# Kernel optimization log

Measured on AMD Instinct MI355X. Metric: run time of the kernel, lower is better.

Reference implementation:

```python
import jax, jax.numpy as jnp
import numpy as np

CAPACITY_FACTOR = 1.25


def setup_inputs() -> dict:
    key = jax.random.key(0)
    ks = jax.random.split(key, 5)
    B, N, D, E, H = 4, 2048, 1024, 8, 4096
    x = jax.random.normal(ks[0], (B, N, D), dtype=jnp.float32)
    w_router = jax.random.normal(ks[1], (D, E), dtype=jnp.float32) * 0.02
    w1 = jax.random.normal(ks[2], (E, D, H), dtype=jnp.float32) * 0.02
    b1 = jnp.zeros((E, H), dtype=jnp.float32)
    w2 = jax.random.normal(ks[3], (E, H, D), dtype=jnp.float32) * 0.02
    b2 = jnp.zeros((E, D), dtype=jnp.float32)
    return {"x": x, "w_router": w_router, "w1": w1, "b1": b1, "w2": w2, "b2": b2}


def reference(x, w_router, w1, b1, w2, b2):
    B, N, D = x.shape
    E = w_router.shape[1]
    C = int(N * CAPACITY_FACTOR // E)  # expert capacity

    # ---- top-1 switch router ----
    logits = jnp.einsum('bnd,de->bne', x, w_router)                 # [B,N,E]
    z = jax.nn.logsumexp(logits, axis=-1)                           # [B,N]
    router_z_loss = jnp.mean(z * z)
    probs = jax.nn.softmax(logits, axis=-1)                         # [B,N,E]
    gate = jnp.max(probs, axis=-1)                                  # [B,N]
    idx = jnp.argmax(probs, axis=-1)                                # [B,N]
    mask = jax.nn.one_hot(idx, E, dtype=x.dtype)                    # [B,N,E]

    # load-balancing aux loss (Switch-Transformer style)
    density = jnp.mean(mask, axis=1)                                # [B,E] fraction routed
    density_proxy = jnp.mean(probs, axis=1)                         # [B,E] mean router prob
    aux_loss = jnp.mean(jnp.sum(density * density_proxy, axis=-1)) * (E * E)

    # position within each expert; drop tokens beyond capacity
    pos = jnp.cumsum(mask, axis=1) - 1.0                            # [B,N,E]
    pos = pos.astype(jnp.int32)
    # one_hot zeros out indices outside [0,C); mask zeros unrouted slots
    dispatch = mask[..., None] * jax.nn.one_hot(pos, C, dtype=x.dtype)  # [B,N,E,C]
    combine = dispatch * gate[:, :, None, None]                     # [B,N,E,C]

    # ---- dense dispatch -> grouped expert FFN -> dense combine ----
    expert_inputs = jnp.einsum('bnd,bnec->becd', x, dispatch)       # [B,E,C,D]
    h = jax.nn.gelu(jnp.einsum('becd,edh->bech', expert_inputs, w1)
                    + b1[None, :, None, :])                          # [B,E,C,H]
    expert_outputs = jnp.einsum('bech,ehd->becd', h, w2) + b2[None, :, None, :]
    output = jnp.einsum('becd,bnec->bnd', expert_outputs, combine)  # [B,N,D]
    return output, aux_loss, router_z_loss
```

## Files before the change

### kernel.cpp

```cpp
#include <hip/hip_runtime.h>
#include <hip/hip_bf16.h>
#include <math.h>

#define B_ 4
#define N_ 2048
#define D_ 1024
#define E_ 8
#define H_ 4096
#define C_ 320
#define M_ (B_*C_)

typedef __attribute__((ext_vector_type(8))) short short8;
typedef __attribute__((ext_vector_type(4))) float floatx4;

__device__ __forceinline__ unsigned short f2bf(float f) {
  unsigned u = __builtin_bit_cast(unsigned, f);
  u += 0x7fffu + ((u >> 16) & 1u);
  return (unsigned short)(u >> 16);
}

__device__ __forceinline__ float gelu_fast(float x) {
  float u = 0.7978845608028654f * (x + 0.044715f * x * x * x);
  float t = 1.f - 2.f / (__expf(2.f * u) + 1.f);
  return 0.5f * x * (1.f + t);
}

__device__ __forceinline__ void gload_lds16(const unsigned short* g, unsigned short* l) {
  __builtin_amdgcn_global_load_lds(
      (const __attribute__((address_space(1))) unsigned int*)g,
      (__attribute__((address_space(3))) unsigned int*)l, 16, 0, 0);
}

__global__ __launch_bounds__(256) void router_kernel(
    const float* __restrict__ x, const float* __restrict__ wr,
    int* __restrict__ idx_buf, float* __restrict__ gate_buf,
    float* __restrict__ stats)
{
  int lane  = threadIdx.x & 63;
  int wave  = threadIdx.x >> 6;
  int token = blockIdx.x * 4 + wave;
  int b     = token >> 11;

  const float* xp = x + (size_t)token * D_ + lane * 16;
  float xv[16];
#pragma unroll
  for (int i = 0; i < 4; i++) {
    float4 v = ((const float4*)xp)[i];
    xv[i*4+0]=v.x; xv[i*4+1]=v.y; xv[i*4+2]=v.z; xv[i*4+3]=v.w;
  }
  double acc[8];
#pragma unroll
  for (int e = 0; e < 8; e++) acc[e] = 0.0;
  const float* wp = wr + (size_t)(lane * 16) * E_;
#pragma unroll
  for (int i = 0; i < 16; i++) {
    float xs = xv[i];
#pragma unroll
    for (int e = 0; e < 8; e++) acc[e] += (double)xs * (double)wp[i*8 + e];
  }
  for (int off = 32; off > 0; off >>= 1) {
#pragma unroll
    for (int e = 0; e < 8; e++) acc[e] += __shfl_xor(acc[e], off, 64);
  }

  float l[8];
#pragma unroll
  for (int e = 0; e < 8; e++) l[e] = (float)acc[e];
  float m = l[0]; int best = 0;
#pragma unroll
  for (int e = 1; e < 8; e++) if (l[e] > m) { m = l[e]; best = e; }
  float p[8], sum = 0.f;
#pragma unroll
  for (int e = 0; e < 8; e++) { p[e] = expf(l[e] - m); sum += p[e]; }
  float inv = 1.f / sum;
#pragma unroll
  for (int e = 0; e < 8; e++) p[e] *= inv;
  float z    = m + logf(sum);
  float gate = inv;

  __shared__ float s_cnt[8], s_prox[8], s_zsq[1];
  if (threadIdx.x < 8)  { s_cnt[threadIdx.x] = 0.f; s_prox[threadIdx.x] = 0.f; }
  if (threadIdx.x == 8) s_zsq[0] = 0.f;
  __syncthreads();
  if (lane == 0) {
    idx_buf[token]  = best;
    gate_buf[token] = gate;
    atomicAdd(&s_zsq[0], z * z);
    atomicAdd(&s_cnt[best], 1.f);
#pragma unroll
    for (int e = 0; e < 8; e++) atomicAdd(&s_prox[e], p[e]);
  }
  __syncthreads();
  if (threadIdx.x < 8) {
    atomicAdd(&stats[b*8 + threadIdx.x],      s_cnt[threadIdx.x]);
    atomicAdd(&stats[32 + b*8 + threadIdx.x], s_prox[threadIdx.x]);
  }
  if (threadIdx.x == 8) atomicAdd(&stats[64], s_zsq[0]);
}

__global__ __launch_bounds__(64) void pos_kernel(
    const int* __restrict__ idx_buf, int* __restrict__ slot_token)
{
  int be = blockIdx.x;
  int b = be >> 3, e = be & 7;
  int lane = threadIdx.x;
  int base = 0;
  int* out = slot_token + (size_t)(e * B_ + b) * C_;
  for (int n0 = 0; n0 < N_; n0 += 64) {
    int n = n0 + lane;
    bool match = (idx_buf[b * N_ + n] == e);
    unsigned long long mask = __ballot(match);
    int my = base + __popcll(mask & ((1ull << lane) - 1ull));
    if (match && my < C_) out[my] = b * N_ + n;
    base += __popcll(mask);
  }
}

__global__ __launch_bounds__(256) void gather_kernel(
    const float* __restrict__ x, const int* __restrict__ slot_token,
    unsigned short* __restrict__ xe)
{
  int row = blockIdx.x;
  int t = slot_token[row];
  int col = threadIdx.x * 4;
  ushort4 o;
  if (t >= 0) {
    float4 v = *(const float4*)(x + (size_t)t * D_ + col);
    o.x = f2bf(v.x); o.y = f2bf(v.y); o.z = f2bf(v.z); o.w = f2bf(v.w);
  } else {
    o.x = 0; o.y = 0; o.z = 0; o.w = 0;
  }
  *(ushort4*)(xe + (size_t)row * D_ + col) = o;
}

__global__ __launch_bounds__(256) void transcast_kernel(
    const float* __restrict__ in, unsigned short* __restrict__ out, int R, int Cc)
{
  int e = blockIdx.z;
  const float* pin = in + (size_t)e * R * Cc;
  unsigned short* pout = out + (size_t)e * R * Cc;
  __shared__ float T[64][65];
  int r0 = blockIdx.y * 64, c0 = blockIdx.x * 64;
  {
    int row = threadIdx.x >> 2;
    int cb  = (threadIdx.x & 3) * 4;
#pragma unroll
    for (int p = 0; p < 4; p++) {
      int col = cb + p * 16;
      float4 v = *(const float4*)(pin + (size_t)(r0 + row) * Cc + c0 + col);
      T[row][col+0] = v.x; T[row][col+1] = v.y; T[row][col+2] = v.z; T[row][col+3] = v.w;
    }
  }
  __syncthreads();
  {
    int ocb = threadIdx.x >> 4;
    int or4 = (threadIdx.x & 15) * 4;
#pragma unroll
    for (int p = 0; p < 4; p++) {
      int oc = ocb + p * 16;
      ushort4 o;
      o.x = f2bf(T[or4+0][oc]); o.y = f2bf(T[or4+1][oc]);
      o.z = f2bf(T[or4+2][oc]); o.w = f2bf(T[or4+3][oc]);
      *(ushort4*)(pout + (size_t)(c0 + oc) * R + r0 + or4) = o;
    }
  }
}

template<int EPI>
__global__ __launch_bounds__(256) void gemm_kernel(
    const unsigned short* __restrict__ A,
    const unsigned short* __restrict__ BT,
    const float* __restrict__ bias,
    unsigned short* __restrict__ Hout,
    float* __restrict__ Out,
    const int* __restrict__ slot_token,
    const float* __restrict__ gate_buf,
    int M, int K, int Nn)
{
  int e  = blockIdx.z;
  int m0 = blockIdx.y * 128;
  int n0 = blockIdx.x * 128;
  const unsigned short* Ae = A  + (size_t)e * M  * K;
  const unsigned short* Be = BT + (size_t)e * Nn * K;

  __shared__ __align__(16) unsigned short As[2][128 * 32];
  __shared__ __align__(16) unsigned short Bs[2][128 * 32];
  __shared__ int   s_tok[128];
  __shared__ float s_gate[128];

  int tid  = threadIdx.x;
  int lane = tid & 63;
  int wave = tid >> 6;
  int wm   = (wave >> 1) * 64;
  int wn   = (wave & 1) * 64;
  int lr   = lane & 15;
  int quad = lane >> 4;

  if constexpr (EPI == 1) {
    if (tid < 128) {
      int t = slot_token[(size_t)e * M + m0 + tid];
      s_tok[tid]  = t;
      s_gate[tid] = (t >= 0) ? gate_buf[t] : 0.f;
    }
  }

  floatx4 acc[4][4];
#pragma unroll
  for (int i = 0; i < 4; i++)
#pragma unroll
    for (int j = 0; j < 4; j++) acc[i][j] = (floatx4){0.f, 0.f, 0.f, 0.f};

  int rA0 = wave * 32 + (lane >> 2);
  int kcc = (lane & 3) * 8;
  const unsigned short* Ag0 = Ae + (size_t)(m0 + rA0)      * K + kcc;
  const unsigned short* Ag1 = Ae + (size_t)(m0 + rA0 + 16) * K + kcc;
  const unsigned short* Bg0 = Be + (size_t)(n0 + rA0)      * K + kcc;
  const unsigned short* Bg1 = Be + (size_t)(n0 + rA0 + 16) * K + kcc;
  const unsigned offA0 = (wave * 32) * 32;
  const unsigned offA1 = (wave * 32 + 16) * 32;

  gload_lds16(Ag0, &As[0][offA0]);
  gload_lds16(Ag1, &As[0][offA1]);
  gload_lds16(Bg0, &Bs[0][offA0]);
  gload_lds16(Bg1, &Bs[0][offA1]);
  Ag0 += 32; Ag1 += 32; Bg0 += 32; Bg1 += 32;

  int nIter = K >> 5;
  int buf = 0;
  for (int it = 0; it < nIter; ++it) {
    __syncthreads();
    if (it + 1 < nIter) {
      gload_lds16(Ag0, &As[buf ^ 1][offA0]);
      gload_lds16(Ag1, &As[buf ^ 1][offA1]);
      gload_lds16(Bg0, &Bs[buf ^ 1][offA0]);
      gload_lds16(Bg1, &Bs[buf ^ 1][offA1]);
      Ag0 += 32; Ag1 += 32; Bg0 += 32; Bg1 += 32;
    }
    short8 af[4], bf[4];
#pragma unroll
    for (int i = 0; i < 4; i++) {
      af[i] = *(const short8*)(&As[buf][(wm + i * 16 + lr) * 32 + quad * 8]);
      bf[i] = *(const short8*)(&Bs[buf][(wn + i * 16 + lr) * 32 + quad * 8]);
    }
#pragma unroll
    for (int i = 0; i < 4; i++)
#pragma unroll
      for (int j = 0; j < 4; j++)
        acc[i][j] = __builtin_amdgcn_mfma_f32_16x16x32_bf16(af[i], bf[j], acc[i][j], 0, 0, 0);
    buf ^= 1;
  }

#pragma unroll
  for (int i = 0; i < 4; i++) {
    int rloc = wm + i * 16 + quad * 4;
#pragma unroll
    for (int j = 0; j < 4; j++) {
      int col = n0 + wn + j * 16 + lr;
      float bz = bias[(size_t)e * Nn + col];
      if constexpr (EPI == 0) {
        size_t base = (size_t)e * M * Nn + (size_t)(m0 + rloc) * Nn + col;
#pragma unroll
        for (int r = 0; r < 4; r++)
          Hout[base + (size_t)r * Nn] = f2bf(gelu_fast(acc[i][j][r] + bz));
      } else {
#pragma unroll
        for (int r = 0; r < 4; r++) {
          int t = s_tok[rloc + r];
          if (t >= 0)
            Out[(size_t)t * D_ + col] = s_gate[rloc + r] * (acc[i][j][r] + bz);
        }
      }
    }
  }
}

__global__ void loss_kernel(const float* __restrict__ stats, float* __restrict__ out)
{
  float aux = 0.f;
  for (int i = 0; i < 32; i++) aux += stats[i] * stats[32 + i];
  aux *= 64.f / ((float)B_ * (float)N_ * (float)N_);
  out[0] = aux;
  out[1] = stats[64] / (float)(B_ * N_);
}

extern "C" void kernel_launch(void* const* d_in, const int* in_sizes, int n_in,
                              void* d_out, int out_size, void* d_ws, size_t ws_size,
                              hipStream_t stream)
{
  (void)in_sizes; (void)n_in; (void)ws_size;
  const float* x  = (const float*)d_in[0];
  const float* wr = (const float*)d_in[1];
  const float* w1 = (const float*)d_in[2];
  const float* b1 = (const float*)d_in[3];
  const float* w2 = (const float*)d_in[4];
  const float* b2 = (const float*)d_in[5];
  float* out = (float*)d_out;

  char* ws = (char*)d_ws;
  int*   idx_buf  = (int*)(ws + 0);
  float* gate_buf = (float*)(ws + 32768);
  float* stats    = (float*)(ws + 65536);
  int*   slot_tok = (int*)(ws + 66560);
  unsigned short* xe  = (unsigned short*)(ws + 107520);
  unsigned short* wbf = (unsigned short*)(ws + 21079040);
  unsigned short* hbf = (unsigned short*)(ws + 88187904);

  hipMemsetAsync(d_out, 0, (size_t)out_size * 4, stream);
  hipMemsetAsync(stats, 0, 1024, stream);
  hipMemsetAsync(slot_tok, 0xFF, (size_t)E_ * B_ * C_ * 4, stream);

  router_kernel<<<(B_ * N_) / 4, 256, 0, stream>>>(x, wr, idx_buf, gate_buf, stats);
  pos_kernel<<<B_ * E_, 64, 0, stream>>>(idx_buf, slot_tok);
  gather_kernel<<<E_ * M_, 256, 0, stream>>>(x, slot_tok, xe);

  transcast_kernel<<<dim3(H_ / 64, D_ / 64, E_), 256, 0, stream>>>(w1, wbf, D_, H_);
  gemm_kernel<0><<<dim3(H_ / 128, M_ / 128, E_), 256, 0, stream>>>(
      xe, wbf, b1, hbf, nullptr, nullptr, nullptr, M_, D_, H_);
  transcast_kernel<<<dim3(D_ / 64, H_ / 64, E_), 256, 0, stream>>>(w2, wbf, H_, D_);
  gemm_kernel<1><<<dim3(D_ / 128, M_ / 128, E_), 256, 0, stream>>>(
      hbf, wbf, b2, nullptr, out, slot_tok, gate_buf, M_, H_, D_);

  loss_kernel<<<1, 1, 0, stream>>>(stats, out + (size_t)B_ * N_ * D_);
}
```

Baseline: 673.4 us.

## Remap GEMM grid to interleave experts and fold loss kernel into pos kernel

The GEMM launches switch from a 3D grid to a flat 1D grid. The expert index is taken from the low bits of blockIdx.x, and M tiles vary fastest within each expert. This changes block dispatch order so that all 8 experts run at once and neighbouring blocks share the same B-weight column tile, which should help L2 reuse of weights and spread work across XCDs. The separate single-thread loss kernel is merged into pos_kernel to save one launch. pos_kernel runs after router_kernel on the same stream, so the stats it reads are already complete.

```diff
diff --git a/kernel.cpp b/kernel.cpp
--- a/kernel.cpp
+++ b/kernel.cpp
@@ -99,7 +99,8 @@
 }
 
 __global__ __launch_bounds__(64) void pos_kernel(
-    const int* __restrict__ idx_buf, int* __restrict__ slot_token)
+    const int* __restrict__ idx_buf, int* __restrict__ slot_token,
+    const float* __restrict__ stats, float* __restrict__ loss_out)
 {
   int be = blockIdx.x;
   int b = be >> 3, e = be & 7;
@@ -114,6 +115,13 @@
     if (match && my < C_) out[my] = b * N_ + n;
     base += __popcll(mask);
   }
+  if (be == 0 && lane == 0) {
+    float aux = 0.f;
+    for (int i = 0; i < 32; i++) aux += stats[i] * stats[32 + i];
+    aux *= 64.f / ((float)B_ * (float)N_ * (float)N_);
+    loss_out[0] = aux;
+    loss_out[1] = stats[64] / (float)(B_ * N_);
+  }
 }
 
 __global__ __launch_bounds__(256) void gather_kernel(
@@ -175,11 +183,12 @@
     float* __restrict__ Out,
     const int* __restrict__ slot_token,
     const float* __restrict__ gate_buf,
-    int M, int K, int Nn)
-{
-  int e  = blockIdx.z;
-  int m0 = blockIdx.y * 128;
-  int n0 = blockIdx.x * 128;
+    int M, int K, int Nn, int MT)
+{
+  int e  = blockIdx.x & 7;
+  int s  = blockIdx.x >> 3;
+  int m0 = (s % MT) * 128;
+  int n0 = (s / MT) * 128;
   const unsigned short* Ae = A  + (size_t)e * M  * K;
   const unsigned short* Be = BT + (size_t)e * Nn * K;
 
@@ -274,15 +283,6 @@
   }
 }
 
-__global__ void loss_kernel(const float* __restrict__ stats, float* __restrict__ out)
-{
-  float aux = 0.f;
-  for (int i = 0; i < 32; i++) aux += stats[i] * stats[32 + i];
-  aux *= 64.f / ((float)B_ * (float)N_ * (float)N_);
-  out[0] = aux;
-  out[1] = stats[64] / (float)(B_ * N_);
-}
-
 extern "C" void kernel_launch(void* const* d_in, const int* in_sizes, int n_in,
                               void* d_out, int out_size, void* d_ws, size_t ws_size,
                               hipStream_t stream)
@@ -310,15 +310,14 @@
   hipMemsetAsync(slot_tok, 0xFF, (size_t)E_ * B_ * C_ * 4, stream);
 
   router_kernel<<<(B_ * N_) / 4, 256, 0, stream>>>(x, wr, idx_buf, gate_buf, stats);
-  pos_kernel<<<B_ * E_, 64, 0, stream>>>(idx_buf, slot_tok);
+  pos_kernel<<<B_ * E_, 64, 0, stream>>>(idx_buf, slot_tok, stats,
+                                         out + (size_t)B_ * N_ * D_);
   gather_kernel<<<E_ * M_, 256, 0, stream>>>(x, slot_tok, xe);
 
   transcast_kernel<<<dim3(H_ / 64, D_ / 64, E_), 256, 0, stream>>>(w1, wbf, D_, H_);
-  gemm_kernel<0><<<dim3(H_ / 128, M_ / 128, E_), 256, 0, stream>>>(
-      xe, wbf, b1, hbf, nullptr, nullptr, nullptr, M_, D_, H_);
+  gemm_kernel<0><<<E_ * (H_ / 128) * (M_ / 128), 256, 0, stream>>>(
+      xe, wbf, b1, hbf, nullptr, nullptr, nullptr, M_, D_, H_, M_ / 128);
   transcast_kernel<<<dim3(D_ / 64, H_ / 64, E_), 256, 0, stream>>>(w2, wbf, H_, D_);
-  gemm_kernel<1><<<dim3(D_ / 128, M_ / 128, E_), 256, 0, stream>>>(
-      hbf, wbf, b2, nullptr, out, slot_tok, gate_buf, M_, H_, D_);
-
-  loss_kernel<<<1, 1, 0, stream>>>(stats, out + (size_t)B_ * N_ * D_);
-}
+  gemm_kernel<1><<<E_ * (D_ / 128) * (M_ / 128), 256, 0, stream>>>(
+      hbf, wbf, b2, nullptr, out, slot_tok, gate_buf, M_, H_, D_, M_ / 128);
+}
```

After: 643.6 us. 1.05x faster.
